# Kernel tuning notes

Hardware: AMD Instinct MI355X
Metric: run time of the kernel (lower is better)

The kernel has to match this reference:

```python
import jax, jax.numpy as jnp
import numpy as np

EMB = 256; HEADS = 8; K = 3; NOBJ = 3; STEPS = 3; MLP = 8; EPS = 1e-5; TEMP = 10000.0


def _pos_enc_2d(bs, h, w, e):
    # PositionalEncodingsFixed: interleaved sin/cos, positions from cumsum (1..h / 1..w)
    d = e // 2
    i = jnp.arange(d, dtype=jnp.float32)
    temp = TEMP ** (2.0 * jnp.floor(i / 2.0) / d)

    def enc1d(pos):  # pos: [n] -> [n, d]
        x = pos[:, None] / temp
        return jnp.stack([jnp.sin(x[:, 0::2]), jnp.cos(x[:, 1::2])], axis=-1).reshape(pos.shape[0], -1)

    ye = enc1d(jnp.arange(1, h + 1, dtype=jnp.float32))  # [h, d]
    xe = enc1d(jnp.arange(1, w + 1, dtype=jnp.float32))  # [w, d]
    pos = jnp.concatenate([
        jnp.broadcast_to(ye[:, None, :], (h, w, d)),
        jnp.broadcast_to(xe[None, :, :], (h, w, d))], axis=-1)  # [h, w, e]
    return jnp.broadcast_to(pos[None], (bs, h, w, e)).transpose(0, 3, 1, 2)  # [bs, e, h, w]


def _ln(x, g, b):
    m = jnp.mean(x, -1, keepdims=True)
    v = jnp.var(x, -1, keepdims=True)
    return (x - m) * jax.lax.rsqrt(v + EPS) * g + b


def _mha(q, k, v, wq, bq, wk, bk, wv, bv, wo, bo):
    # q: [L, B, E], k/v: [S, B, E] (batch_first=False convention)
    L, B, E = q.shape; S = k.shape[0]; Dh = E // HEADS
    qp = (q @ wq + bq).reshape(L, B, HEADS, Dh)
    kp = (k @ wk + bk).reshape(S, B, HEADS, Dh)
    vp = (v @ wv + bv).reshape(S, B, HEADS, Dh)
    att = jax.nn.softmax(jnp.einsum('lbhd,sbhd->bhls', qp, kp) / jnp.sqrt(jnp.float32(Dh)), axis=-1)
    out = jnp.einsum('bhls,sbhd->lbhd', att, vp).reshape(L, B, E)
    return out @ wo + bo


def _forward(f_e, pos_emb, bboxes, shape_map, mha_wq, mha_bq, mha_wk, mha_bk, mha_wv, mha_bv,
             mha_wo, mha_bo, la_wq, la_bq, la_wk, la_bk, la_wv, la_bv,
             ff_w1, ff_b1, ff_w2, ff_b2, n1_g, n1_b, n2_g, n2_b, n3_g, n3_b):
    bs, E, h, w = f_e.shape
    N = NOBJ * K * K
    scale = E ** -0.5
    # shape_emb: [N, bs, E] (zero-shot branch: learned parameter expanded over batch)
    shape_emb = jnp.broadcast_to(shape_map[None], (bs, NOBJ, K * K, E)).reshape(bs, N, E).transpose(1, 0, 2)
    qpe = _pos_enc_2d(bs, K, K, E).reshape(bs, E, K * K).transpose(2, 0, 1)  # [K^2, bs, E]
    query_pos = jnp.tile(qpe, (NOBJ, 1, 1))  # [N, bs, E]
    memory = f_e.reshape(bs, E, h * w).transpose(2, 0, 1).reshape(-1, E)  # [HW*bs, E]
    pos_flat = pos_emb.reshape(-1, E)
    qp_flat = query_pos.reshape(-1, E)

    # LinearAttention k/v paths are loop-invariant; hoist (same math as the per-step recompute).
    kk = jax.nn.softmax((memory + pos_flat) @ la_wk + la_bk, axis=0)  # softmax over rows
    vv = memory @ la_wv + la_bv
    context = jnp.sum(kk * vv, axis=0)  # einsum('be,be->e')

    F_k = shape_emb
    protos = []
    for _ in range(STEPS):
        # 1) cross-attn to shape embeddings (post-norm)
        a = _mha(F_k + query_pos, shape_emb, shape_emb,
                 mha_wq, mha_bq, mha_wk, mha_bk, mha_wv, mha_bv, mha_wo, mha_bo)
        F_k = _ln(F_k + a, n1_g, n1_b)
        # 2) linear attention over image memory
        q = jax.nn.softmax(((F_k.reshape(-1, E) + qp_flat) @ la_wq + la_bq) * scale, axis=-1)
        la = (q * context).reshape(F_k.shape)
        F_k = _ln(F_k + la, n2_g, n2_b)
        # 3) FFN
        ff = jax.nn.gelu(F_k @ ff_w1 + ff_b1, approximate=False) @ ff_w2 + ff_b2
        F_k = _ln(F_k + ff, n3_g, n3_b)
        protos.append(F_k)
    return jnp.stack(protos)  # [STEPS, N, bs, E]


def setup_inputs() -> dict:
    key = jax.random.key(0)
    ks = jax.random.split(key, 24)
    bs, h, w = 32, 64, 64
    s = 0.02
    def n(k, shp, sc=s):
        return jax.random.normal(k, shp, jnp.float32) * sc
    E, F = EMB, MLP * EMB
    return {
        'f_e': jax.random.normal(ks[0], (bs, E, h, w), jnp.float32),
        'pos_emb': jax.random.normal(ks[1], (h * w, bs, E), jnp.float32),
        'bboxes': jax.random.uniform(ks[2], (bs, NOBJ, 4), jnp.float32),
        'shape_map': jax.random.normal(ks[3], (NOBJ, K * K, E), jnp.float32),
        'mha_wq': n(ks[4], (E, E)), 'mha_bq': jnp.zeros(E, jnp.float32),
        'mha_wk': n(ks[5], (E, E)), 'mha_bk': jnp.zeros(E, jnp.float32),
        'mha_wv': n(ks[6], (E, E)), 'mha_bv': jnp.zeros(E, jnp.float32),
        'mha_wo': n(ks[7], (E, E)), 'mha_bo': jnp.zeros(E, jnp.float32),
        'la_wq': n(ks[8], (E, E)), 'la_bq': jnp.zeros(E, jnp.float32),
        'la_wk': n(ks[9], (E, E)), 'la_bk': jnp.zeros(E, jnp.float32),
        'la_wv': n(ks[10], (E, E)), 'la_bv': jnp.zeros(E, jnp.float32),
        'ff_w1': n(ks[11], (E, F)), 'ff_b1': jnp.zeros(F, jnp.float32),
        'ff_w2': n(ks[12], (F, E)), 'ff_b2': jnp.zeros(E, jnp.float32),
        'n1_g': jnp.ones(E, jnp.float32), 'n1_b': jnp.zeros(E, jnp.float32),
        'n2_g': jnp.ones(E, jnp.float32), 'n2_b': jnp.zeros(E, jnp.float32),
        'n3_g': jnp.ones(E, jnp.float32), 'n3_b': jnp.zeros(E, jnp.float32),
    }


def reference(f_e, pos_emb, bboxes, shape_map, mha_wq, mha_bq, mha_wk, mha_bk, mha_wv, mha_bv,
              mha_wo, mha_bo, la_wq, la_bq, la_wk, la_bk, la_wv, la_bv,
              ff_w1, ff_b1, ff_w2, ff_b2, n1_g, n1_b, n2_g, n2_b, n3_g, n3_b):
    return _forward(f_e, pos_emb, bboxes, shape_map, mha_wq, mha_bq, mha_wk, mha_bk, mha_wv, mha_bv,
                    mha_wo, mha_bo, la_wq, la_bq, la_wk, la_bk, la_wv, la_bv,
                    ff_w1, ff_b1, ff_w2, ff_b2, n1_g, n1_b, n2_g, n2_b, n3_g, n3_b)
```

## Files before the change

kernel.cpp:

```cpp
#include <hip/hip_runtime.h>
#include <math.h>

#define EPS_ 1e-5f

#define WS_PART   ((size_t)0)
#define WS_CTX    ((size_t)524288)
#define WS_QP     ((size_t)524544)
#define WS_KP     ((size_t)531456)
#define WS_VP     ((size_t)538368)
#define WS_F      ((size_t)545280)
#define WS_ATTN   ((size_t)766464)
#define WS_H      ((size_t)987648)
#define WS_WKB    ((size_t)1872384)
#define WS_WVB    ((size_t)1905152)
#define WS_WOT    ((size_t)1937920)
#define WS_LAQT   ((size_t)1970688)
#define WS_W1T    ((size_t)2003456)
#define WS_W2T    ((size_t)2265600)
#define WS_MT     ((size_t)2527744)
#define WS_VPT    ((size_t)2560512)
#define WS_CST    ((size_t)2564608)

typedef short bf16x8 __attribute__((ext_vector_type(8)));
typedef float f32x4 __attribute__((ext_vector_type(4)));

__device__ __forceinline__ unsigned short f2bf(float f) {
    union { float f; unsigned u; } v; v.f = f;
    unsigned u = v.u;
    unsigned r = u + 0x7fffu + ((u >> 16) & 1u);
    return (unsigned short)(r >> 16);
}
__device__ __forceinline__ float bf2f(unsigned short s) {
    union { unsigned u; float f; } v; v.u = ((unsigned)s) << 16;
    return v.f;
}
__device__ __forceinline__ bf16x8 cvt8(const float* p) {
    float4 u = ((const float4*)p)[0];
    float4 v = ((const float4*)p)[1];
    bf16x8 r;
    r[0] = (short)f2bf(u.x); r[1] = (short)f2bf(u.y);
    r[2] = (short)f2bf(u.z); r[3] = (short)f2bf(u.w);
    r[4] = (short)f2bf(v.x); r[5] = (short)f2bf(v.y);
    r[6] = (short)f2bf(v.z); r[7] = (short)f2bf(v.w);
    return r;
}
__device__ __forceinline__ bf16x8 cvt8sum(const float* p, const float* q) {
    float4 u = ((const float4*)p)[0];
    float4 v = ((const float4*)p)[1];
    float4 a = ((const float4*)q)[0];
    float4 b = ((const float4*)q)[1];
    bf16x8 r;
    r[0] = (short)f2bf(u.x + a.x); r[1] = (short)f2bf(u.y + a.y);
    r[2] = (short)f2bf(u.z + a.z); r[3] = (short)f2bf(u.w + a.w);
    r[4] = (short)f2bf(v.x + b.x); r[5] = (short)f2bf(v.y + b.y);
    r[6] = (short)f2bf(v.z + b.z); r[7] = (short)f2bf(v.w + b.w);
    return r;
}

__global__ __launch_bounds__(256) void k_trans(const float* __restrict__ la_wk,
                                               const float* __restrict__ la_wv,
                                               const float* __restrict__ mha_wo,
                                               const float* __restrict__ la_wq,
                                               const float* __restrict__ ff_w1,
                                               const float* __restrict__ ff_w2,
                                               unsigned short* __restrict__ wkb,
                                               unsigned short* __restrict__ wvb,
                                               unsigned short* __restrict__ woT,
                                               unsigned short* __restrict__ laqT,
                                               unsigned short* __restrict__ w1T,
                                               unsigned short* __restrict__ w2T) {
    __shared__ float T[64][65];
    int id = blockIdx.x, t = threadIdx.x;
    const float* src; unsigned short* dst; int R, C, tr, tc;
    if (id < 64) {
        int task = id >> 4, tile = id & 15;
        R = 256; C = 256; tr = tile >> 2; tc = tile & 3;
        src = task == 0 ? la_wk : task == 1 ? la_wv : task == 2 ? mha_wo : la_wq;
        dst = task == 0 ? wkb : task == 1 ? wvb : task == 2 ? woT : laqT;
    } else if (id < 192) {
        int tile = id - 64;
        R = 256; C = 2048; tr = tile >> 5; tc = tile & 31;
        src = ff_w1; dst = w1T;
    } else {
        int tile = id - 192;
        R = 2048; C = 256; tr = tile >> 2; tc = tile & 3;
        src = ff_w2; dst = w2T;
    }
    int r0 = tr * 64, c0 = tc * 64;
    int i = t >> 2, j0 = (t & 3) * 16;
    const float* s = src + (size_t)(r0 + i) * C + c0 + j0;
#pragma unroll
    for (int k = 0; k < 4; ++k) {
        float4 v = ((const float4*)s)[k];
        T[i][j0 + 4 * k + 0] = v.x;
        T[i][j0 + 4 * k + 1] = v.y;
        T[i][j0 + 4 * k + 2] = v.z;
        T[i][j0 + 4 * k + 3] = v.w;
    }
    __syncthreads();
    unsigned short o[16];
#pragma unroll
    for (int k = 0; k < 16; ++k) o[k] = f2bf(T[j0 + k][i]);
    unsigned short* d = dst + (size_t)(c0 + i) * R + r0 + j0;
    ((uint4*)d)[0] = *(const uint4*)&o[0];
    ((uint4*)d)[1] = *(const uint4*)&o[8];
}

__global__ __launch_bounds__(256, 2) void pa_gemm(const float* __restrict__ f_e,
                                                  const float* __restrict__ pos_emb,
                                                  const unsigned short* __restrict__ wkb,
                                                  const unsigned short* __restrict__ wvb,
                                                  const float* __restrict__ bk,
                                                  const float* __restrict__ bv,
                                                  float* __restrict__ part) {
    __shared__ __align__(16) unsigned short lv[2][128 * 40];
    __shared__ float reds[2 * 128];
    __shared__ float redt[2 * 128];

    const int g  = blockIdx.x;
    const int et = g & 1;
    const int pt = (g >> 1) & 31;
    const int b  = g >> 6;
    const int p0 = pt * 128;
    const int e0 = et * 128;

    const int tid  = threadIdx.x;
    const int wave = tid >> 6;
    const int lane = tid & 63;
    const int quad = lane >> 4;
    const int l15  = lane & 15;
    const int wm = wave >> 1;
    const int wn = wave & 1;

    f32x4 accx[4][4], accv[4][4];
    const f32x4 zero4 = {0.f, 0.f, 0.f, 0.f};
#pragma unroll
    for (int i = 0; i < 4; ++i)
#pragma unroll
        for (int j = 0; j < 4; ++j) { accx[i][j] = zero4; accv[i][j] = zero4; }

    const int sk  = tid >> 3;
    const int sm0 = (tid & 7) << 4;

    const float* feb = f_e + (size_t)b * (256 * 4096) + p0;
    const float* posb = pos_emb + ((size_t)(p0 + wm * 64 + l15) * 32 + b) * 256 + quad * 8;
    const unsigned short* wkp = wkb + (size_t)(e0 + wn * 64 + l15) * 256 + quad * 8;
    const unsigned short* wvp = wvb + (size_t)(e0 + wn * 64 + l15) * 256 + quad * 8;

    float4 pf[4];
    {
        const float* src = feb + (size_t)sk * 4096 + sm0;
#pragma unroll
        for (int i = 0; i < 4; ++i) pf[i] = ((const float4*)src)[i];
    }

#pragma unroll 1
    for (int kt = 0; kt < 8; ++kt) {
        const int c0 = kt * 32;
        unsigned short* L = lv[kt & 1];
#pragma unroll
        for (int i = 0; i < 4; ++i) {
            L[(sm0 + 4 * i + 0) * 40 + sk] = f2bf(pf[i].x);
            L[(sm0 + 4 * i + 1) * 40 + sk] = f2bf(pf[i].y);
            L[(sm0 + 4 * i + 2) * 40 + sk] = f2bf(pf[i].z);
            L[(sm0 + 4 * i + 3) * 40 + sk] = f2bf(pf[i].w);
        }
        float4 nf[4];
        if (kt < 7) {
            const float* src = feb + (size_t)(c0 + 32 + sk) * 4096 + sm0;
#pragma unroll
            for (int i = 0; i < 4; ++i) nf[i] = ((const float4*)src)[i];
        }
        float4 pp[4][2];
#pragma unroll
        for (int ms = 0; ms < 4; ++ms) {
            const float* p = posb + (size_t)ms * (16 * 32 * 256) + c0;
            pp[ms][0] = ((const float4*)p)[0];
            pp[ms][1] = ((const float4*)p)[1];
        }
        __syncthreads();
        bf16x8 fk[4], fv[4];
#pragma unroll
        for (int ns = 0; ns < 4; ++ns) {
            fk[ns] = *(const bf16x8*)(wkp + (size_t)ns * (16 * 256) + c0);
            fv[ns] = *(const bf16x8*)(wvp + (size_t)ns * (16 * 256) + c0);
        }
#pragma unroll
        for (int ms = 0; ms < 4; ++ms) {
            int row = wm * 64 + ms * 16 + l15;
            uint4 avu = *(const uint4*)&L[row * 40 + quad * 8];
            bf16x8 av = *(const bf16x8*)&avu;
            bf16x8 ax;
            ax[0] = (short)f2bf(__uint_as_float(avu.x << 16)          + pp[ms][0].x);
            ax[1] = (short)f2bf(__uint_as_float(avu.x & 0xffff0000u)  + pp[ms][0].y);
            ax[2] = (short)f2bf(__uint_as_float(avu.y << 16)          + pp[ms][0].z);
            ax[3] = (short)f2bf(__uint_as_float(avu.y & 0xffff0000u)  + pp[ms][0].w);
            ax[4] = (short)f2bf(__uint_as_float(avu.z << 16)          + pp[ms][1].x);
            ax[5] = (short)f2bf(__uint_as_float(avu.z & 0xffff0000u)  + pp[ms][1].y);
            ax[6] = (short)f2bf(__uint_as_float(avu.w << 16)          + pp[ms][1].z);
            ax[7] = (short)f2bf(__uint_as_float(avu.w & 0xffff0000u)  + pp[ms][1].w);
#pragma unroll
            for (int ns = 0; ns < 4; ++ns) {
                accx[ms][ns] = __builtin_amdgcn_mfma_f32_16x16x32_bf16(ax, fk[ns], accx[ms][ns], 0, 0, 0);
                accv[ms][ns] = __builtin_amdgcn_mfma_f32_16x16x32_bf16(av, fv[ns], accv[ms][ns], 0, 0, 0);
            }
        }
        if (kt < 7) {
#pragma unroll
            for (int i = 0; i < 4; ++i) pf[i] = nf[i];
        }
    }

#pragma unroll
    for (int ns = 0; ns < 4; ++ns) {
        int nloc = wn * 64 + ns * 16 + l15;
        float bkv = bk[e0 + nloc];
        float bvv = bv[e0 + nloc];
        float ps = 0.f, pt_ = 0.f;
#pragma unroll
        for (int ms = 0; ms < 4; ++ms)
#pragma unroll
            for (int r = 0; r < 4; ++r) {
                float ex = __expf(accx[ms][ns][r] + bkv);
                float vv = accv[ms][ns][r] + bvv;
                ps += ex;
                pt_ += ex * vv;
            }
        ps  += __shfl_xor(ps, 16);  ps  += __shfl_xor(ps, 32);
        pt_ += __shfl_xor(pt_, 16); pt_ += __shfl_xor(pt_, 32);
        if (lane < 16) { reds[wm * 128 + nloc] = ps; redt[wm * 128 + nloc] = pt_; }
    }
    __syncthreads();
    if (tid < 128) {
        float s = reds[tid] + reds[128 + tid];
        float t = redt[tid] + redt[128 + tid];
        part[(size_t)g * 256 + tid] = s;
        part[(size_t)g * 256 + 128 + tid] = t;
    }
}

__global__ __launch_bounds__(256) void pa_reduce(const float* __restrict__ part,
                                                 float* __restrict__ ctx) {
    int e = blockIdx.x, tid = threadIdx.x;
    int et = e >> 7, n = e & 127;
    float s = 0.f, t = 0.f;
#pragma unroll
    for (int j = 0; j < 4; ++j) {
        int q = tid * 4 + j;
        const float* p = part + (size_t)(q * 2 + et) * 256 + n;
        s += p[0];
        t += p[128];
    }
    int wave = tid >> 6, lane = tid & 63;
#pragma unroll
    for (int o = 1; o < 64; o <<= 1) { s += __shfl_xor(s, o); t += __shfl_xor(t, o); }
    __shared__ float rs[4], rt[4];
    if (lane == 0) { rs[wave] = s; rt[wave] = t; }
    __syncthreads();
    if (tid == 0) {
        float S = rs[0] + rs[1] + rs[2] + rs[3];
        float T = rt[0] + rt[1] + rt[2] + rt[3];
        ctx[e] = T / S;
    }
}

__global__ __launch_bounds__(256) void k_qpos(float* __restrict__ qp) {
    int n = blockIdx.x, e = threadIdx.x;
    int q9 = n % 9;
    int y = q9 / 3, x = q9 % 3;
    float pos; int idx;
    if (e < 128) { pos = (float)(y + 1); idx = e; }
    else         { pos = (float)(x + 1); idx = e - 128; }
    int j = idx >> 1;
    float inv = expf(-(float)j * 0.14391156831212787f);
    float arg = pos * inv;
    qp[(size_t)n * 256 + e] = (idx & 1) ? cosf(arg) : sinf(arg);
}

__global__ __launch_bounds__(256) void k_kvproj(const float* __restrict__ sm,
                                                const float* __restrict__ wk,
                                                const float* __restrict__ bk,
                                                const float* __restrict__ wv,
                                                const float* __restrict__ bv,
                                                float* __restrict__ kp,
                                                float* __restrict__ vp) {
    int g = blockIdx.x;
    int n = g % 27, which = g / 27;
    int e = threadIdx.x;
    const float* W = which ? wv : wk;
    const float* B = which ? bv : bk;
    float* O = which ? vp : kp;
    const float* row = sm + (size_t)n * 256;
    float acc = 0.f;
    for (int c = 0; c < 256; ++c) acc += row[c] * W[(size_t)c * 256 + e];
    O[(size_t)n * 256 + e] = acc + B[e];
}

__global__ __launch_bounds__(256) void k_mt(const float* __restrict__ wq,
                                            const float* __restrict__ bq,
                                            const float* __restrict__ kp,
                                            unsigned short* __restrict__ MT,
                                            float* __restrict__ cst) {
    int h = blockIdx.x >> 5, s = blockIdx.x & 31;
    int c = threadIdx.x;
    const float SC = 0.17677669529663687f;
    if (s < 27) {
        float a = 0.f;
#pragma unroll
        for (int d = 0; d < 32; ++d)
            a += wq[(size_t)c * 256 + h * 32 + d] * kp[(size_t)s * 256 + h * 32 + d];
        MT[((size_t)(h * 32 + s)) * 256 + c] = f2bf(a * SC);
        if (c == 0) {
            float cb = 0.f;
#pragma unroll
            for (int d = 0; d < 32; ++d) cb += bq[h * 32 + d] * kp[(size_t)s * 256 + h * 32 + d];
            cst[h * 32 + s] = cb * SC;
        }
    } else {
        MT[((size_t)(h * 32 + s)) * 256 + c] = 0;
        if (c == 0) cst[h * 32 + s] = -1e30f;
    }
}

__global__ __launch_bounds__(256) void k_vpt(const float* __restrict__ vp,
                                             unsigned short* __restrict__ vpT) {
    int h = blockIdx.x, t = threadIdx.x;
    int s = t & 31;
#pragma unroll
    for (int i = 0; i < 4; ++i) {
        int d = (t >> 5) + 8 * i;
        vpT[((size_t)(h * 32 + d)) * 32 + s] = (s < 27) ? f2bf(vp[(size_t)s * 256 + h * 32 + d]) : (unsigned short)0;
    }
}

__global__ __launch_bounds__(256) void k_finit(const float* __restrict__ sm,
                                               float* __restrict__ F) {
    int r = blockIdx.x, e = threadIdx.x;
    F[(size_t)r * 256 + e] = sm[(size_t)(r >> 5) * 256 + e];
}

__global__ __launch_bounds__(256) void b1_attn(const float* __restrict__ F,
                                               const float* __restrict__ qp,
                                               const unsigned short* __restrict__ MT,
                                               const float* __restrict__ cst,
                                               const unsigned short* __restrict__ vpT,
                                               float* __restrict__ aout) {
    __shared__ float S[32][33];
    __shared__ __align__(16) unsigned short Pb[32][40];
    int b = blockIdx.x >> 3, h = blockIdx.x & 7;
    int tid = threadIdx.x, wave = tid >> 6, lane = tid & 63;
    int quad = lane >> 4, l15 = lane & 15;
    int lt = wave >> 1, st = wave & 1;
    const f32x4 z4 = {0.f, 0.f, 0.f, 0.f};
    f32x4 acc = z4;
    int l = lt * 16 + l15;
    bool lok = (l < 27);
    const float* xF = F + (size_t)(l * 32 + b) * 256;
    const float* xq = qp + (size_t)l * 256;
    const unsigned short* Bp = MT + (size_t)(h * 32 + st * 16 + l15) * 256;
#pragma unroll
    for (int kt = 0; kt < 8; ++kt) {
        int c = kt * 32 + quad * 8;
        bf16x8 a;
        if (lok) a = cvt8sum(xF + c, xq + c);
        else {
#pragma unroll
            for (int i = 0; i < 8; ++i) a[i] = 0;
        }
        bf16x8 bb = *(const bf16x8*)(Bp + c);
        acc = __builtin_amdgcn_mfma_f32_16x16x32_bf16(a, bb, acc, 0, 0, 0);
    }
    float cstv = cst[h * 32 + st * 16 + l15];
#pragma unroll
    for (int r = 0; r < 4; ++r) S[lt * 16 + quad * 4 + r][st * 16 + l15] = acc[r] + cstv;
    __syncthreads();
    if (tid < 32) {
        float pv[32];
        float m = -1e30f;
#pragma unroll
        for (int s = 0; s < 32; ++s) { pv[s] = S[tid][s]; m = fmaxf(m, pv[s]); }
        float sum = 0.f;
#pragma unroll
        for (int s = 0; s < 32; ++s) { pv[s] = __expf(pv[s] - m); sum += pv[s]; }
        float inv = 1.f / sum;
#pragma unroll
        for (int s = 0; s < 32; ++s) Pb[tid][s] = f2bf(pv[s] * inv);
    }
    __syncthreads();
    bf16x8 a2 = *(const bf16x8*)&Pb[lt * 16 + l15][quad * 8];
    bf16x8 b2 = *(const bf16x8*)(vpT + (size_t)(h * 32 + st * 16 + l15) * 32 + quad * 8);
    f32x4 o = __builtin_amdgcn_mfma_f32_16x16x32_bf16(a2, b2, z4, 0, 0, 0);
#pragma unroll
    for (int r = 0; r < 4; ++r) {
        int ll = lt * 16 + quad * 4 + r;
        if (ll < 27) aout[(size_t)(ll * 32 + b) * 256 + h * 32 + st * 16 + l15] = o[r];
    }
}

__global__ __launch_bounds__(256) void b2_mid(const float* __restrict__ aout,
                                              const unsigned short* __restrict__ woT,
                                              const float* __restrict__ bo,
                                              float* __restrict__ F,
                                              const float* __restrict__ g1,
                                              const float* __restrict__ b1v,
                                              const float* __restrict__ qp,
                                              const unsigned short* __restrict__ laqT,
                                              const float* __restrict__ labq,
                                              const float* __restrict__ ctx,
                                              const float* __restrict__ g2,
                                              const float* __restrict__ b2v) {
    __shared__ __align__(16) unsigned short X1b[16][264];
    __shared__ float r1s[4][16], r1q[4][16], rm[4][16], rp[4][16], r2s[4][16], r2q[4][16];
    int r0 = blockIdx.x * 16;
    int lrow = r0 >> 5;
    int tid = threadIdx.x, w = tid >> 6, lane = tid & 63;
    int quad = lane >> 4, l15 = lane & 15;
    const f32x4 z4 = {0.f, 0.f, 0.f, 0.f};
    f32x4 acc[4] = {z4, z4, z4, z4};
    const float* Ap = aout + (size_t)(r0 + l15) * 256;
#pragma unroll
    for (int kt = 0; kt < 8; ++kt) {
        int c = kt * 32 + quad * 8;
        bf16x8 a = cvt8(Ap + c);
#pragma unroll
        for (int nt = 0; nt < 4; ++nt) {
            bf16x8 bb = *(const bf16x8*)(woT + (size_t)(w * 64 + nt * 16 + l15) * 256 + c);
            acc[nt] = __builtin_amdgcn_mfma_f32_16x16x32_bf16(a, bb, acc[nt], 0, 0, 0);
        }
    }
    int e_[4];
#pragma unroll
    for (int nt = 0; nt < 4; ++nt) e_[nt] = w * 64 + nt * 16 + l15;
    float val[4][4];
#pragma unroll
    for (int nt = 0; nt < 4; ++nt) {
        float bov = bo[e_[nt]];
#pragma unroll
        for (int r = 0; r < 4; ++r) {
            int row = quad * 4 + r;
            val[nt][r] = acc[nt][r] + bov + F[(size_t)(r0 + row) * 256 + e_[nt]];
        }
    }
#pragma unroll
    for (int r = 0; r < 4; ++r) {
        float s = val[0][r] + val[1][r] + val[2][r] + val[3][r];
        float q = val[0][r] * val[0][r] + val[1][r] * val[1][r] + val[2][r] * val[2][r] + val[3][r] * val[3][r];
#pragma unroll
        for (int o = 1; o < 16; o <<= 1) { s += __shfl_xor(s, o); q += __shfl_xor(q, o); }
        if (l15 == 0) { r1s[w][quad * 4 + r] = s; r1q[w][quad * 4 + r] = q; }
    }
    __syncthreads();
#pragma unroll
    for (int r = 0; r < 4; ++r) {
        int row = quad * 4 + r;
        float S = r1s[0][row] + r1s[1][row] + r1s[2][row] + r1s[3][row];
        float Q = r1q[0][row] + r1q[1][row] + r1q[2][row] + r1q[3][row];
        float mean = S * (1.f / 256.f);
        float var  = Q * (1.f / 256.f) - mean * mean;
        float rs   = rsqrtf(var + EPS_);
#pragma unroll
        for (int nt = 0; nt < 4; ++nt) {
            int e = e_[nt];
            float f1 = (val[nt][r] - mean) * rs * g1[e] + b1v[e];
            X1b[row][e] = f2bf(f1 + qp[(size_t)lrow * 256 + e]);
            val[nt][r] = f1;
        }
    }
    __syncthreads();
    f32x4 acc2[4] = {z4, z4, z4, z4};
#pragma unroll
    for (int kt = 0; kt < 8; ++kt) {
        int c = kt * 32 + quad * 8;
        bf16x8 a = *(const bf16x8*)&X1b[l15][c];
#pragma unroll
        for (int nt = 0; nt < 4; ++nt) {
            bf16x8 bb = *(const bf16x8*)(laqT + (size_t)(w * 64 + nt * 16 + l15) * 256 + c);
            acc2[nt] = __builtin_amdgcn_mfma_f32_16x16x32_bf16(a, bb, acc2[nt], 0, 0, 0);
        }
    }
    float y[4][4];
#pragma unroll
    for (int nt = 0; nt < 4; ++nt) {
        float bqv = labq[e_[nt]];
#pragma unroll
        for (int r = 0; r < 4; ++r) y[nt][r] = (acc2[nt][r] + bqv) * 0.0625f;
    }
#pragma unroll
    for (int r = 0; r < 4; ++r) {
        float m = fmaxf(fmaxf(y[0][r], y[1][r]), fmaxf(y[2][r], y[3][r]));
#pragma unroll
        for (int o = 1; o < 16; o <<= 1) m = fmaxf(m, __shfl_xor(m, o));
        if (l15 == 0) rm[w][quad * 4 + r] = m;
    }
    __syncthreads();
    float p[4][4];
#pragma unroll
    for (int r = 0; r < 4; ++r) {
        int row = quad * 4 + r;
        float M = fmaxf(fmaxf(rm[0][row], rm[1][row]), fmaxf(rm[2][row], rm[3][row]));
        float ps = 0.f;
#pragma unroll
        for (int nt = 0; nt < 4; ++nt) { p[nt][r] = __expf(y[nt][r] - M); ps += p[nt][r]; }
#pragma unroll
        for (int o = 1; o < 16; o <<= 1) ps += __shfl_xor(ps, o);
        if (l15 == 0) rp[w][row] = ps;
    }
    __syncthreads();
#pragma unroll
    for (int r = 0; r < 4; ++r) {
        int row = quad * 4 + r;
        float Ssum = rp[0][row] + rp[1][row] + rp[2][row] + rp[3][row];
        float inv = 1.f / Ssum;
#pragma unroll
        for (int nt = 0; nt < 4; ++nt)
            val[nt][r] = val[nt][r] + (p[nt][r] * inv) * ctx[e_[nt]];
    }
#pragma unroll
    for (int r = 0; r < 4; ++r) {
        float s = val[0][r] + val[1][r] + val[2][r] + val[3][r];
        float q = val[0][r] * val[0][r] + val[1][r] * val[1][r] + val[2][r] * val[2][r] + val[3][r] * val[3][r];
#pragma unroll
        for (int o = 1; o < 16; o <<= 1) { s += __shfl_xor(s, o); q += __shfl_xor(q, o); }
        if (l15 == 0) { r2s[w][quad * 4 + r] = s; r2q[w][quad * 4 + r] = q; }
    }
    __syncthreads();
#pragma unroll
    for (int r = 0; r < 4; ++r) {
        int row = quad * 4 + r;
        float S = r2s[0][row] + r2s[1][row] + r2s[2][row] + r2s[3][row];
        float Q = r2q[0][row] + r2q[1][row] + r2q[2][row] + r2q[3][row];
        float mean = S * (1.f / 256.f);
        float var  = Q * (1.f / 256.f) - mean * mean;
        float rs   = rsqrtf(var + EPS_);
#pragma unroll
        for (int nt = 0; nt < 4; ++nt) {
            int e = e_[nt];
            F[(size_t)(r0 + row) * 256 + e] = (val[nt][r] - mean) * rs * g2[e] + b2v[e];
        }
    }
}

__global__ __launch_bounds__(256) void b3_ffn1(const float* __restrict__ F,
                                               const unsigned short* __restrict__ w1T,
                                               const float* __restrict__ fb1,
                                               unsigned short* __restrict__ Hb) {
    int bm = blockIdx.x >> 5, bn = blockIdx.x & 31;
    int tid = threadIdx.x, w = tid >> 6, lane = tid & 63;
    int quad = lane >> 4, l15 = lane & 15;
    int r0 = bm * 16;
    int n0 = bn * 64 + w * 16;
    const f32x4 z4 = {0.f, 0.f, 0.f, 0.f};
    f32x4 acc = z4;
    const float* Ap = F + (size_t)(r0 + l15) * 256;
    const unsigned short* Bp = w1T + (size_t)(n0 + l15) * 256;
#pragma unroll
    for (int kt = 0; kt < 8; ++kt) {
        int c = kt * 32 + quad * 8;
        bf16x8 a = cvt8(Ap + c);
        bf16x8 bb = *(const bf16x8*)(Bp + c);
        acc = __builtin_amdgcn_mfma_f32_16x16x32_bf16(a, bb, acc, 0, 0, 0);
    }
    int e = n0 + l15;
    float bv = fb1[e];
#pragma unroll
    for (int r = 0; r < 4; ++r) {
        float hh = acc[r] + bv;
        float g = 0.5f * hh * (1.f + erff(hh * 0.70710678118654752f));
        Hb[(size_t)(r0 + quad * 4 + r) * 2048 + e] = f2bf(g);
    }
}

__global__ __launch_bounds__(256) void b4_ffn2(const unsigned short* __restrict__ Hb,
                                               const unsigned short* __restrict__ w2T,
                                               const float* __restrict__ fb2,
                                               float* __restrict__ F,
                                               const float* __restrict__ g3,
                                               const float* __restrict__ b3v,
                                               float* __restrict__ out,
                                               int step) {
    __shared__ float r3s[4][16], r3q[4][16];
    int r0 = blockIdx.x * 16;
    int tid = threadIdx.x, w = tid >> 6, lane = tid & 63;
    int quad = lane >> 4, l15 = lane & 15;
    const f32x4 z4 = {0.f, 0.f, 0.f, 0.f};
    f32x4 acc[4] = {z4, z4, z4, z4};
    const unsigned short* Ap = Hb + (size_t)(r0 + l15) * 2048;
#pragma unroll 4
    for (int kt = 0; kt < 64; ++kt) {
        int c = kt * 32 + quad * 8;
        bf16x8 a = *(const bf16x8*)(Ap + c);
#pragma unroll
        for (int nt = 0; nt < 4; ++nt) {
            bf16x8 bb = *(const bf16x8*)(w2T + (size_t)(w * 64 + nt * 16 + l15) * 2048 + c);
            acc[nt] = __builtin_amdgcn_mfma_f32_16x16x32_bf16(a, bb, acc[nt], 0, 0, 0);
        }
    }
    int e_[4];
#pragma unroll
    for (int nt = 0; nt < 4; ++nt) e_[nt] = w * 64 + nt * 16 + l15;
    float val[4][4];
#pragma unroll
    for (int nt = 0; nt < 4; ++nt) {
        float bv = fb2[e_[nt]];
#pragma unroll
        for (int r = 0; r < 4; ++r) {
            int row = quad * 4 + r;
            val[nt][r] = acc[nt][r] + bv + F[(size_t)(r0 + row) * 256 + e_[nt]];
        }
    }
#pragma unroll
    for (int r = 0; r < 4; ++r) {
        float s = val[0][r] + val[1][r] + val[2][r] + val[3][r];
        float q = val[0][r] * val[0][r] + val[1][r] * val[1][r] + val[2][r] * val[2][r] + val[3][r] * val[3][r];
#pragma unroll
        for (int o = 1; o < 16; o <<= 1) { s += __shfl_xor(s, o); q += __shfl_xor(q, o); }
        if (l15 == 0) { r3s[w][quad * 4 + r] = s; r3q[w][quad * 4 + r] = q; }
    }
    __syncthreads();
#pragma unroll
    for (int r = 0; r < 4; ++r) {
        int row = quad * 4 + r;
        float S = r3s[0][row] + r3s[1][row] + r3s[2][row] + r3s[3][row];
        float Q = r3q[0][row] + r3q[1][row] + r3q[2][row] + r3q[3][row];
        float mean = S * (1.f / 256.f);
        float var  = Q * (1.f / 256.f) - mean * mean;
        float rs   = rsqrtf(var + EPS_);
#pragma unroll
        for (int nt = 0; nt < 4; ++nt) {
            int e = e_[nt];
            float o = (val[nt][r] - mean) * rs * g3[e] + b3v[e];
            F[(size_t)(r0 + row) * 256 + e] = o;
            out[(size_t)step * 221184 + (size_t)(r0 + row) * 256 + e] = o;
        }
    }
}

extern "C" void kernel_launch(void* const* d_in, const int* in_sizes, int n_in,
                              void* d_out, int out_size, void* d_ws, size_t ws_size,
                              hipStream_t stream) {
    const float* f_e     = (const float*)d_in[0];
    const float* pos_emb = (const float*)d_in[1];
    const float* sm      = (const float*)d_in[3];
    const float* mha_wq  = (const float*)d_in[4];
    const float* mha_bq  = (const float*)d_in[5];
    const float* mha_wk  = (const float*)d_in[6];
    const float* mha_bk  = (const float*)d_in[7];
    const float* mha_wv  = (const float*)d_in[8];
    const float* mha_bv  = (const float*)d_in[9];
    const float* mha_wo  = (const float*)d_in[10];
    const float* mha_bo  = (const float*)d_in[11];
    const float* la_wq   = (const float*)d_in[12];
    const float* la_bq   = (const float*)d_in[13];
    const float* la_wk   = (const float*)d_in[14];
    const float* la_bk   = (const float*)d_in[15];
    const float* la_wv   = (const float*)d_in[16];
    const float* la_bv   = (const float*)d_in[17];
    const float* ff_w1   = (const float*)d_in[18];
    const float* ff_b1   = (const float*)d_in[19];
    const float* ff_w2   = (const float*)d_in[20];
    const float* ff_b2   = (const float*)d_in[21];
    const float* n1_g    = (const float*)d_in[22];
    const float* n1_b    = (const float*)d_in[23];
    const float* n2_g    = (const float*)d_in[24];
    const float* n2_b    = (const float*)d_in[25];
    const float* n3_g    = (const float*)d_in[26];
    const float* n3_b    = (const float*)d_in[27];

    float* ws = (float*)d_ws;
    float* part = ws + WS_PART;
    float* ctx  = ws + WS_CTX;
    float* qp   = ws + WS_QP;
    float* kp   = ws + WS_KP;
    float* vp   = ws + WS_VP;
    float* F    = ws + WS_F;
    float* aout = ws + WS_ATTN;
    unsigned short* Hb   = (unsigned short*)(ws + WS_H);
    unsigned short* wkb  = (unsigned short*)(ws + WS_WKB);
    unsigned short* wvb  = (unsigned short*)(ws + WS_WVB);
    unsigned short* woT  = (unsigned short*)(ws + WS_WOT);
    unsigned short* laqT = (unsigned short*)(ws + WS_LAQT);
    unsigned short* w1T  = (unsigned short*)(ws + WS_W1T);
    unsigned short* w2T  = (unsigned short*)(ws + WS_W2T);
    unsigned short* MT   = (unsigned short*)(ws + WS_MT);
    unsigned short* vpT  = (unsigned short*)(ws + WS_VPT);
    float* cst = ws + WS_CST;

    float* out = (float*)d_out;

    k_trans<<<320, 256, 0, stream>>>(la_wk, la_wv, mha_wo, la_wq, ff_w1, ff_w2,
                                     wkb, wvb, woT, laqT, w1T, w2T);
    k_qpos<<<27, 256, 0, stream>>>(qp);
    k_kvproj<<<54, 256, 0, stream>>>(sm, mha_wk, mha_bk, mha_wv, mha_bv, kp, vp);
    k_mt<<<256, 256, 0, stream>>>(mha_wq, mha_bq, kp, MT, cst);
    k_vpt<<<8, 256, 0, stream>>>(vp, vpT);
    k_finit<<<864, 256, 0, stream>>>(sm, F);

    pa_gemm<<<2048, 256, 0, stream>>>(f_e, pos_emb, wkb, wvb, la_bk, la_bv, part);
    pa_reduce<<<256, 256, 0, stream>>>(part, ctx);

    for (int s = 0; s < 3; ++s) {
        b1_attn<<<256, 256, 0, stream>>>(F, qp, MT, cst, vpT, aout);
        b2_mid<<<54, 256, 0, stream>>>(aout, woT, mha_bo, F, n1_g, n1_b, qp,
                                       laqT, la_bq, ctx, n2_g, n2_b);
        b3_ffn1<<<1728, 256, 0, stream>>>(F, w1T, ff_b1, Hb);
        b4_ffn2<<<54, 256, 0, stream>>>(Hb, w2T, ff_b2, F, n3_g, n3_b, out, s);
    }
}
```

Measured before the change: 743.0 us.

## Vectorize LDS staging of features and prefetch positional embeddings one step ahead

Changes the feature-tile staging so each thread loads float2 pairs across 8 channels and writes two packed 16-byte bf16 rows to LDS, replacing 16 scalar LDS stores per thread. Positional-embedding loads are now issued one k-step ahead inside the MFMA loop. The __syncthreads is replaced by an explicit lgkmcnt wait plus s_barrier, so outstanding global prefetches are not forced to complete at the barrier. The aim is to cut LDS store count and hide global load latency, at the cost of more live registers.

```diff
diff --git a/kernel.cpp b/kernel.cpp
--- a/kernel.cpp
+++ b/kernel.cpp
@@ -139,75 +139,81 @@
 #pragma unroll
         for (int j = 0; j < 4; ++j) { accx[i][j] = zero4; accv[i][j] = zero4; }
 
-    const int sk  = tid >> 3;
-    const int sm0 = (tid & 7) << 4;
-
-    const float* feb = f_e + (size_t)b * (256 * 4096) + p0;
+    const int pp = tid & 63;
+    const int cg = tid >> 6;
+
+    const float* feb  = f_e + (size_t)b * (256 * 4096) + p0 + 2 * pp;
     const float* posb = pos_emb + ((size_t)(p0 + wm * 64 + l15) * 32 + b) * 256 + quad * 8;
     const unsigned short* wkp = wkb + (size_t)(e0 + wn * 64 + l15) * 256 + quad * 8;
     const unsigned short* wvp = wvb + (size_t)(e0 + wn * 64 + l15) * 256 + quad * 8;
 
-    float4 pf[4];
-    {
-        const float* src = feb + (size_t)sk * 4096 + sm0;
-#pragma unroll
-        for (int i = 0; i < 4; ++i) pf[i] = ((const float4*)src)[i];
+    float2 nf[8];
+#pragma unroll
+    for (int j = 0; j < 8; ++j)
+        nf[j] = *(const float2*)(feb + (size_t)(8 * cg + j) * 4096);
+    float4 npp[4][2];
+#pragma unroll
+    for (int ms = 0; ms < 4; ++ms) {
+        const float* p = posb + (size_t)ms * (16 * 32 * 256);
+        npp[ms][0] = ((const float4*)p)[0];
+        npp[ms][1] = ((const float4*)p)[1];
     }
 
 #pragma unroll 1
     for (int kt = 0; kt < 8; ++kt) {
         const int c0 = kt * 32;
         unsigned short* L = lv[kt & 1];
-#pragma unroll
-        for (int i = 0; i < 4; ++i) {
-            L[(sm0 + 4 * i + 0) * 40 + sk] = f2bf(pf[i].x);
-            L[(sm0 + 4 * i + 1) * 40 + sk] = f2bf(pf[i].y);
-            L[(sm0 + 4 * i + 2) * 40 + sk] = f2bf(pf[i].z);
-            L[(sm0 + 4 * i + 3) * 40 + sk] = f2bf(pf[i].w);
-        }
-        float4 nf[4];
-        if (kt < 7) {
-            const float* src = feb + (size_t)(c0 + 32 + sk) * 4096 + sm0;
-#pragma unroll
-            for (int i = 0; i < 4; ++i) nf[i] = ((const float4*)src)[i];
-        }
-        float4 pp[4][2];
-#pragma unroll
-        for (int ms = 0; ms < 4; ++ms) {
-            const float* p = posb + (size_t)ms * (16 * 32 * 256) + c0;
-            pp[ms][0] = ((const float4*)p)[0];
-            pp[ms][1] = ((const float4*)p)[1];
-        }
-        __syncthreads();
+
+        {
+            bf16x8 lo, hi;
+#pragma unroll
+            for (int j = 0; j < 8; ++j) {
+                lo[j] = (short)f2bf(nf[j].x);
+                hi[j] = (short)f2bf(nf[j].y);
+            }
+            *(bf16x8*)&L[(2 * pp)     * 40 + 8 * cg] = lo;
+            *(bf16x8*)&L[(2 * pp + 1) * 40 + 8 * cg] = hi;
+        }
         bf16x8 fk[4], fv[4];
 #pragma unroll
         for (int ns = 0; ns < 4; ++ns) {
             fk[ns] = *(const bf16x8*)(wkp + (size_t)ns * (16 * 256) + c0);
             fv[ns] = *(const bf16x8*)(wvp + (size_t)ns * (16 * 256) + c0);
         }
+        if (kt < 7) {
+#pragma unroll
+            for (int j = 0; j < 8; ++j)
+                nf[j] = *(const float2*)(feb + (size_t)(c0 + 32 + 8 * cg + j) * 4096);
+        }
+        asm volatile("s_waitcnt lgkmcnt(0)" ::: "memory");
+        __builtin_amdgcn_s_barrier();
+        asm volatile("" ::: "memory");
+
 #pragma unroll
         for (int ms = 0; ms < 4; ++ms) {
+            float4 q0 = npp[ms][0], q1 = npp[ms][1];
+            if (kt < 7) {
+                const float* p = posb + (size_t)ms * (16 * 32 * 256) + c0 + 32;
+                npp[ms][0] = ((const float4*)p)[0];
+                npp[ms][1] = ((const float4*)p)[1];
+            }
             int row = wm * 64 + ms * 16 + l15;
             uint4 avu = *(const uint4*)&L[row * 40 + quad * 8];
             bf16x8 av = *(const bf16x8*)&avu;
             bf16x8 ax;
-            ax[0] = (short)f2bf(__uint_as_float(avu.x << 16)          + pp[ms][0].x);
-            ax[1] = (short)f2bf(__uint_as_float(avu.x & 0xffff0000u)  + pp[ms][0].y);
-            ax[2] = (short)f2bf(__uint_as_float(avu.y << 16)          + pp[ms][0].z);
-            ax[3] = (short)f2bf(__uint_as_float(avu.y & 0xffff0000u)  + pp[ms][0].w);
-            ax[4] = (short)f2bf(__uint_as_float(avu.z << 16)          + pp[ms][1].x);
-            ax[5] = (short)f2bf(__uint_as_float(avu.z & 0xffff0000u)  + pp[ms][1].y);
-            ax[6] = (short)f2bf(__uint_as_float(avu.w << 16)          + pp[ms][1].z);
-            ax[7] = (short)f2bf(__uint_as_float(avu.w & 0xffff0000u)  + pp[ms][1].w);
+            ax[0] = (short)f2bf(__uint_as_float(avu.x << 16)          + q0.x);
+            ax[1] = (short)f2bf(__uint_as_float(avu.x & 0xffff0000u)  + q0.y);
+            ax[2] = (short)f2bf(__uint_as_float(avu.y << 16)          + q0.z);
+            ax[3] = (short)f2bf(__uint_as_float(avu.y & 0xffff0000u)  + q0.w);
+            ax[4] = (short)f2bf(__uint_as_float(avu.z << 16)          + q1.x);
+            ax[5] = (short)f2bf(__uint_as_float(avu.z & 0xffff0000u)  + q1.y);
+            ax[6] = (short)f2bf(__uint_as_float(avu.w << 16)          + q1.z);
+            ax[7] = (short)f2bf(__uint_as_float(avu.w & 0xffff0000u)  + q1.w);
 #pragma unroll
             for (int ns = 0; ns < 4; ++ns) {
                 accx[ms][ns] = __builtin_amdgcn_mfma_f32_16x16x32_bf16(ax, fk[ns], accx[ms][ns], 0, 0, 0);
                 accv[ms][ns] = __builtin_amdgcn_mfma_f32_16x16x32_bf16(av, fv[ns], accv[ms][ns], 0, 0, 0);
             }
-        }
-        if (kt < 7) {
-#pragma unroll
-            for (int i = 0; i < 4; ++i) pf[i] = nf[i];
         }
     }
 
```

Result: no change. 729.3 us (-1.9%).

## Register double-buffer pa_gemm without LDS and merge small setup kernels

Applied to the files above, without the earlier changes.

The pa_gemm kernel drops its LDS staging and barrier. Each wave now loads f_e, pos_emb and weight fragments straight into registers, using two register sets that alternate so loads overlap with MFMA work. It also uses 512 threads per block with half the M-tile per wave and hardware packed bf16 conversion. The tiny setup kernels (qpos, finit, vpt) are folded into k_trans and k_mt to cut launch count. The per-thread f_e loads are now strided scalars rather than float4 vectors, and the doubled register sets add register pressure, either of which could reduce efficiency.

```diff
diff --git a/kernel.cpp b/kernel.cpp
--- a/kernel.cpp
+++ b/kernel.cpp
@@ -68,9 +68,30 @@
                                                unsigned short* __restrict__ woT,
                                                unsigned short* __restrict__ laqT,
                                                unsigned short* __restrict__ w1T,
-                                               unsigned short* __restrict__ w2T) {
+                                               unsigned short* __restrict__ w2T,
+                                               const float* __restrict__ sm,
+                                               float* __restrict__ F,
+                                               float* __restrict__ qp) {
     __shared__ float T[64][65];
     int id = blockIdx.x, t = threadIdx.x;
+    if (id >= 347) {
+        int r = id - 347;
+        F[(size_t)r * 256 + t] = sm[(size_t)(r >> 5) * 256 + t];
+        return;
+    }
+    if (id >= 320) {
+        int n = id - 320, e = t;
+        int q9 = n % 9;
+        int y = q9 / 3, x = q9 % 3;
+        float pos; int idx;
+        if (e < 128) { pos = (float)(y + 1); idx = e; }
+        else         { pos = (float)(x + 1); idx = e - 128; }
+        int j = idx >> 1;
+        float inv = expf(-(float)j * 0.14391156831212787f);
+        float arg = pos * inv;
+        qp[(size_t)n * 256 + e] = (idx & 1) ? cosf(arg) : sinf(arg);
+        return;
+    }
     const float* src; unsigned short* dst; int R, C, tr, tc;
     if (id < 64) {
         int task = id >> 4, tile = id & 15;
@@ -106,16 +127,58 @@
     ((uint4*)d)[1] = *(const uint4*)&o[8];
 }
 
-__global__ __launch_bounds__(256, 2) void pa_gemm(const float* __restrict__ f_e,
+#define PA_LOAD(FE, PQ, WK, WV, KT)                                           \
+    do {                                                                      \
+        const int kt_ = (KT);                                                 \
+        _Pragma("unroll") for (int ms = 0; ms < 2; ++ms) {                    \
+            _Pragma("unroll") for (int j = 0; j < 8; ++j)                     \
+                FE[ms][j] = fe0[(size_t)(kt_ * 32 + j) * 4096 + ms * 16];     \
+            const float* pp_ = pos0 + (size_t)ms * (16 * 32 * 256) + kt_ * 32;\
+            PQ[ms][0] = ((const float4*)pp_)[0];                              \
+            PQ[ms][1] = ((const float4*)pp_)[1];                              \
+        }                                                                     \
+        _Pragma("unroll") for (int ns = 0; ns < 4; ++ns) {                    \
+            WK[ns] = *(const bf16x8*)(wk0 + (size_t)ns * (16 * 256) + kt_ * 32);\
+            WV[ns] = *(const bf16x8*)(wv0 + (size_t)ns * (16 * 256) + kt_ * 32);\
+        }                                                                     \
+    } while (0)
+
+#define PA_COMP(FE, PQ, WK, WV)                                               \
+    do {                                                                      \
+        _Pragma("unroll") for (int ms = 0; ms < 2; ++ms) {                    \
+            float fx0 = FE[ms][0] + PQ[ms][0].x;                              \
+            float fx1 = FE[ms][1] + PQ[ms][0].y;                              \
+            float fx2 = FE[ms][2] + PQ[ms][0].z;                              \
+            float fx3 = FE[ms][3] + PQ[ms][0].w;                              \
+            float fx4 = FE[ms][4] + PQ[ms][1].x;                              \
+            float fx5 = FE[ms][5] + PQ[ms][1].y;                              \
+            float fx6 = FE[ms][6] + PQ[ms][1].z;                              \
+            float fx7 = FE[ms][7] + PQ[ms][1].w;                              \
+            union { unsigned u[4]; bf16x8 v; } av_, ax_;                      \
+            asm("v_cvt_pk_bf16_f32 %0, %1, %2" : "=v"(av_.u[0]) : "v"(FE[ms][0]), "v"(FE[ms][1])); \
+            asm("v_cvt_pk_bf16_f32 %0, %1, %2" : "=v"(av_.u[1]) : "v"(FE[ms][2]), "v"(FE[ms][3])); \
+            asm("v_cvt_pk_bf16_f32 %0, %1, %2" : "=v"(av_.u[2]) : "v"(FE[ms][4]), "v"(FE[ms][5])); \
+            asm("v_cvt_pk_bf16_f32 %0, %1, %2" : "=v"(av_.u[3]) : "v"(FE[ms][6]), "v"(FE[ms][7])); \
+            asm("v_cvt_pk_bf16_f32 %0, %1, %2" : "=v"(ax_.u[0]) : "v"(fx0), "v"(fx1)); \
+            asm("v_cvt_pk_bf16_f32 %0, %1, %2" : "=v"(ax_.u[1]) : "v"(fx2), "v"(fx3)); \
+            asm("v_cvt_pk_bf16_f32 %0, %1, %2" : "=v"(ax_.u[2]) : "v"(fx4), "v"(fx5)); \
+            asm("v_cvt_pk_bf16_f32 %0, %1, %2" : "=v"(ax_.u[3]) : "v"(fx6), "v"(fx7)); \
+            _Pragma("unroll") for (int ns = 0; ns < 4; ++ns) {                \
+                accx[ms][ns] = __builtin_amdgcn_mfma_f32_16x16x32_bf16(ax_.v, WK[ns], accx[ms][ns], 0, 0, 0); \
+                accv[ms][ns] = __builtin_amdgcn_mfma_f32_16x16x32_bf16(av_.v, WV[ns], accv[ms][ns], 0, 0, 0); \
+            }                                                                 \
+        }                                                                     \
+    } while (0)
+
+__global__ __launch_bounds__(512, 2) void pa_gemm(const float* __restrict__ f_e,
                                                   const float* __restrict__ pos_emb,
                                                   const unsigned short* __restrict__ wkb,
                                                   const unsigned short* __restrict__ wvb,
                                                   const float* __restrict__ bk,
                                                   const float* __restrict__ bv,
                                                   float* __restrict__ part) {
-    __shared__ __align__(16) unsigned short lv[2][128 * 40];
-    __shared__ float reds[2 * 128];
-    __shared__ float redt[2 * 128];
+    __shared__ float reds[4][128];
+    __shared__ float redt[4][128];
 
     const int g  = blockIdx.x;
     const int et = g & 1;
@@ -132,83 +195,30 @@
     const int wm = wave >> 1;
     const int wn = wave & 1;
 
-    f32x4 accx[4][4], accv[4][4];
+    f32x4 accx[2][4], accv[2][4];
     const f32x4 zero4 = {0.f, 0.f, 0.f, 0.f};
 #pragma unroll
-    for (int i = 0; i < 4; ++i)
+    for (int i = 0; i < 2; ++i)
 #pragma unroll
         for (int j = 0; j < 4; ++j) { accx[i][j] = zero4; accv[i][j] = zero4; }
 
-    const int sk  = tid >> 3;
-    const int sm0 = (tid & 7) << 4;
-
-    const float* feb = f_e + (size_t)b * (256 * 4096) + p0;
-    const float* posb = pos_emb + ((size_t)(p0 + wm * 64 + l15) * 32 + b) * 256 + quad * 8;
-    const unsigned short* wkp = wkb + (size_t)(e0 + wn * 64 + l15) * 256 + quad * 8;
-    const unsigned short* wvp = wvb + (size_t)(e0 + wn * 64 + l15) * 256 + quad * 8;
-
-    float4 pf[4];
-    {
-        const float* src = feb + (size_t)sk * 4096 + sm0;
-#pragma unroll
-        for (int i = 0; i < 4; ++i) pf[i] = ((const float4*)src)[i];
-    }
+    const float* fe0  = f_e + ((size_t)b * 256 + quad * 8) * 4096 + (p0 + wm * 32 + l15);
+    const float* pos0 = pos_emb + ((size_t)(p0 + wm * 32 + l15) * 32 + b) * 256 + quad * 8;
+    const unsigned short* wk0 = wkb + (size_t)(e0 + wn * 64 + l15) * 256 + quad * 8;
+    const unsigned short* wv0 = wvb + (size_t)(e0 + wn * 64 + l15) * 256 + quad * 8;
+
+    float  feA[2][8], feB[2][8];
+    float4 pqA[2][2], pqB[2][2];
+    bf16x8 wkA[4], wkB[4], wvA[4], wvB[4];
+
+    PA_LOAD(feA, pqA, wkA, wvA, 0);
 
 #pragma unroll 1
-    for (int kt = 0; kt < 8; ++kt) {
-        const int c0 = kt * 32;
-        unsigned short* L = lv[kt & 1];
-#pragma unroll
-        for (int i = 0; i < 4; ++i) {
-            L[(sm0 + 4 * i + 0) * 40 + sk] = f2bf(pf[i].x);
-            L[(sm0 + 4 * i + 1) * 40 + sk] = f2bf(pf[i].y);
-            L[(sm0 + 4 * i + 2) * 40 + sk] = f2bf(pf[i].z);
-            L[(sm0 + 4 * i + 3) * 40 + sk] = f2bf(pf[i].w);
-        }
-        float4 nf[4];
-        if (kt < 7) {
-            const float* src = feb + (size_t)(c0 + 32 + sk) * 4096 + sm0;
-#pragma unroll
-            for (int i = 0; i < 4; ++i) nf[i] = ((const float4*)src)[i];
-        }
-        float4 pp[4][2];
-#pragma unroll
-        for (int ms = 0; ms < 4; ++ms) {
-            const float* p = posb + (size_t)ms * (16 * 32 * 256) + c0;
-            pp[ms][0] = ((const float4*)p)[0];
-            pp[ms][1] = ((const float4*)p)[1];
-        }
-        __syncthreads();
-        bf16x8 fk[4], fv[4];
-#pragma unroll
-        for (int ns = 0; ns < 4; ++ns) {
-            fk[ns] = *(const bf16x8*)(wkp + (size_t)ns * (16 * 256) + c0);
-            fv[ns] = *(const bf16x8*)(wvp + (size_t)ns * (16 * 256) + c0);
-        }
-#pragma unroll
-        for (int ms = 0; ms < 4; ++ms) {
-            int row = wm * 64 + ms * 16 + l15;
-            uint4 avu = *(const uint4*)&L[row * 40 + quad * 8];
-            bf16x8 av = *(const bf16x8*)&avu;
-            bf16x8 ax;
-            ax[0] = (short)f2bf(__uint_as_float(avu.x << 16)          + pp[ms][0].x);
-            ax[1] = (short)f2bf(__uint_as_float(avu.x & 0xffff0000u)  + pp[ms][0].y);
-            ax[2] = (short)f2bf(__uint_as_float(avu.y << 16)          + pp[ms][0].z);
-            ax[3] = (short)f2bf(__uint_as_float(avu.y & 0xffff0000u)  + pp[ms][0].w);
-            ax[4] = (short)f2bf(__uint_as_float(avu.z << 16)          + pp[ms][1].x);
-            ax[5] = (short)f2bf(__uint_as_float(avu.z & 0xffff0000u)  + pp[ms][1].y);
-            ax[6] = (short)f2bf(__uint_as_float(avu.w << 16)          + pp[ms][1].z);
-            ax[7] = (short)f2bf(__uint_as_float(avu.w & 0xffff0000u)  + pp[ms][1].w);
-#pragma unroll
-            for (int ns = 0; ns < 4; ++ns) {
-                accx[ms][ns] = __builtin_amdgcn_mfma_f32_16x16x32_bf16(ax, fk[ns], accx[ms][ns], 0, 0, 0);
-                accv[ms][ns] = __builtin_amdgcn_mfma_f32_16x16x32_bf16(av, fv[ns], accv[ms][ns], 0, 0, 0);
-            }
-        }
-        if (kt < 7) {
-#pragma unroll
-            for (int i = 0; i < 4; ++i) pf[i] = nf[i];
-        }
+    for (int ktp = 0; ktp < 4; ++ktp) {
+        PA_LOAD(feB, pqB, wkB, wvB, 2 * ktp + 1);
+        PA_COMP(feA, pqA, wkA, wvA);
+        if (ktp < 3) PA_LOAD(feA, pqA, wkA, wvA, 2 * ktp + 2);
+        PA_COMP(feB, pqB, wkB, wvB);
     }
 
 #pragma unroll
@@ -218,7 +228,7 @@
         float bvv = bv[e0 + nloc];
         float ps = 0.f, pt_ = 0.f;
 #pragma unroll
-        for (int ms = 0; ms < 4; ++ms)
+        for (int ms = 0; ms < 2; ++ms)
 #pragma unroll
             for (int r = 0; r < 4; ++r) {
                 float ex = __expf(accx[ms][ns][r] + bkv);
@@ -228,12 +238,12 @@
             }
         ps  += __shfl_xor(ps, 16);  ps  += __shfl_xor(ps, 32);
         pt_ += __shfl_xor(pt_, 16); pt_ += __shfl_xor(pt_, 32);
-        if (lane < 16) { reds[wm * 128 + nloc] = ps; redt[wm * 128 + nloc] = pt_; }
+        if (lane < 16) { reds[wm][nloc] = ps; redt[wm][nloc] = pt_; }
     }
     __syncthreads();
     if (tid < 128) {
-        float s = reds[tid] + reds[128 + tid];
-        float t = redt[tid] + redt[128 + tid];
+        float s = reds[0][tid] + reds[1][tid] + reds[2][tid] + reds[3][tid];
+        float t = redt[0][tid] + redt[1][tid] + redt[2][tid] + redt[3][tid];
         part[(size_t)g * 256 + tid] = s;
         part[(size_t)g * 256 + 128 + tid] = t;
     }
@@ -262,19 +272,6 @@
         float T = rt[0] + rt[1] + rt[2] + rt[3];
         ctx[e] = T / S;
     }
-}
-
-__global__ __launch_bounds__(256) void k_qpos(float* __restrict__ qp) {
-    int n = blockIdx.x, e = threadIdx.x;
-    int q9 = n % 9;
-    int y = q9 / 3, x = q9 % 3;
-    float pos; int idx;
-    if (e < 128) { pos = (float)(y + 1); idx = e; }
-    else         { pos = (float)(x + 1); idx = e - 128; }
-    int j = idx >> 1;
-    float inv = expf(-(float)j * 0.14391156831212787f);
-    float arg = pos * inv;
-    qp[(size_t)n * 256 + e] = (idx & 1) ? cosf(arg) : sinf(arg);
 }
 
 __global__ __launch_bounds__(256) void k_kvproj(const float* __restrict__ sm,
@@ -299,8 +296,20 @@
 __global__ __launch_bounds__(256) void k_mt(const float* __restrict__ wq,
                                             const float* __restrict__ bq,
                                             const float* __restrict__ kp,
+                                            const float* __restrict__ vp,
                                             unsigned short* __restrict__ MT,
+                                            unsigned short* __restrict__ vpT,
                                             float* __restrict__ cst) {
+    if (blockIdx.x >= 256) {
+        int h = blockIdx.x - 256, t = threadIdx.x;
+        int s = t & 31;
+#pragma unroll
+        for (int i = 0; i < 4; ++i) {
+            int d = (t >> 5) + 8 * i;
+            vpT[((size_t)(h * 32 + d)) * 32 + s] = (s < 27) ? f2bf(vp[(size_t)s * 256 + h * 32 + d]) : (unsigned short)0;
+        }
+        return;
+    }
     int h = blockIdx.x >> 5, s = blockIdx.x & 31;
     int c = threadIdx.x;
     const float SC = 0.17677669529663687f;
@@ -320,23 +329,6 @@
         MT[((size_t)(h * 32 + s)) * 256 + c] = 0;
         if (c == 0) cst[h * 32 + s] = -1e30f;
     }
-}
-
-__global__ __launch_bounds__(256) void k_vpt(const float* __restrict__ vp,
-                                             unsigned short* __restrict__ vpT) {
-    int h = blockIdx.x, t = threadIdx.x;
-    int s = t & 31;
-#pragma unroll
-    for (int i = 0; i < 4; ++i) {
-        int d = (t >> 5) + 8 * i;
-        vpT[((size_t)(h * 32 + d)) * 32 + s] = (s < 27) ? f2bf(vp[(size_t)s * 256 + h * 32 + d]) : (unsigned short)0;
-    }
-}
-
-__global__ __launch_bounds__(256) void k_finit(const float* __restrict__ sm,
-                                               float* __restrict__ F) {
-    int r = blockIdx.x, e = threadIdx.x;
-    F[(size_t)r * 256 + e] = sm[(size_t)(r >> 5) * 256 + e];
 }
 
 __global__ __launch_bounds__(256) void b1_attn(const float* __restrict__ F,
@@ -687,15 +679,12 @@
 
     float* out = (float*)d_out;
 
-    k_trans<<<320, 256, 0, stream>>>(la_wk, la_wv, mha_wo, la_wq, ff_w1, ff_w2,
-                                     wkb, wvb, woT, laqT, w1T, w2T);
-    k_qpos<<<27, 256, 0, stream>>>(qp);
+    k_trans<<<1211, 256, 0, stream>>>(la_wk, la_wv, mha_wo, la_wq, ff_w1, ff_w2,
+                                      wkb, wvb, woT, laqT, w1T, w2T, sm, F, qp);
     k_kvproj<<<54, 256, 0, stream>>>(sm, mha_wk, mha_bk, mha_wv, mha_bv, kp, vp);
-    k_mt<<<256, 256, 0, stream>>>(mha_wq, mha_bq, kp, MT, cst);
-    k_vpt<<<8, 256, 0, stream>>>(vp, vpT);
-    k_finit<<<864, 256, 0, stream>>>(sm, F);
-
-    pa_gemm<<<2048, 256, 0, stream>>>(f_e, pos_emb, wkb, wvb, la_bk, la_bv, part);
+    k_mt<<<264, 256, 0, stream>>>(mha_wq, mha_bq, kp, vp, MT, vpT, cst);
+
+    pa_gemm<<<2048, 512, 0, stream>>>(f_e, pos_emb, wkb, wvb, la_bk, la_bv, part);
     pa_reduce<<<256, 256, 0, stream>>>(part, ctx);
 
     for (int s = 0; s < 3; ++s) {
```

Result: slower. 810.1 us (+9.0%).
